# Kernel optimization log

Hardware: AMD Instinct MI355X
Metric: run time of the kernel (lower is better)

Reference implementation:

```python
import jax, jax.numpy as jnp
import numpy as np

ROW = COL = 8   # unfold tile size
KS = 5          # gaussian raster kernel size
C1 = 6          # high-freq feature split

def conv2d(x, w, b=None, pad=0):
    y = jax.lax.conv_general_dilated(x, w, (1, 1), [(pad, pad), (pad, pad)],
                                     dimension_numbers=('NCHW', 'OIHW', 'NCHW'))
    if b is not None:
        y = y + b[None, :, None, None]
    return y

def unfold_tiles(x, r, c):
    # non-overlapping Unfold(kernel=(r,c), stride=(r,c)) -> [B*L, C, r, c]
    B, C, H, W = x.shape
    x = x.reshape(B, C, H // r, r, W // c, c).transpose(0, 2, 4, 1, 3, 5)
    return x.reshape(B * (H // r) * (W // c), C, r, c)

def fold_tiles(t, B, C, H, W, r, c):
    t = t.reshape(B, H // r, W // c, C, r, c).transpose(0, 3, 1, 4, 2, 5)
    return t.reshape(B, C, H, W)

def setup_inputs() -> dict:
    key = jax.random.key(0)
    ks = jax.random.split(key, 16)
    B, NF, H, W, P = 32, 48, 128, 128, 81
    inp = {
        'ms': jax.random.normal(ks[0], (B, 4, 32, 32), jnp.float32),
        'feat': jax.random.normal(ks[1], (B, NF, H, W), jnp.float32),
        'V': jax.random.normal(ks[2], (B, NF, H, W), jnp.float32),
        'logits_raw': jax.random.normal(ks[3], (B, P, H, W), jnp.float32),
        'sigma_x': jax.random.uniform(ks[4], (P,), jnp.float32, 0.2, 3.0),
        'sigma_y': jax.random.uniform(ks[5], (P,), jnp.float32, 0.2, 3.0),
        'opacity': jax.random.uniform(ks[6], (P,), jnp.float32, 0.1, 1.0),
        'rho': jax.random.uniform(ks[7], (P,), jnp.float32, -0.9, 0.9),
        'w_v2': jax.random.normal(ks[8], (42, 42, 1, 1), jnp.float32) * 0.05,
        'w_fine': jax.random.normal(ks[9], (4, NF, 3, 3), jnp.float32) * 0.05,
        'b_fine': jax.random.normal(ks[10], (4,), jnp.float32) * 0.05,
        'w_res': jax.random.normal(ks[11], (4, NF, 1, 1), jnp.float32) * 0.05,
        'b_res': jax.random.normal(ks[12], (4,), jnp.float32) * 0.05,
    }
    return inp

def reference(ms, feat, V, logits_raw, sigma_x, sigma_y, opacity, rho,
              w_v2, w_fine, b_fine, w_res, b_res):
    B, nf, H, W = feat.shape
    # soft class assignment (gumbel_softmax tau=1, zero-noise deterministic surrogate)
    logits = jax.nn.softmax(logits_raw, axis=1)
    feat1, lr_feat = feat[:, :C1], feat[:, C1:]
    V1, V2 = V[:, :C1], V[:, C1:]
    # H,W are already multiples of ROW/COL -> bicubic-to-same-size is identity
    uf = unfold_tiles(feat1, ROW, COL)        # [B*L, c1, 8, 8]
    ul = unfold_tiles(logits, ROW, COL)       # [B*L, P, 8, 8]
    uv1 = unfold_tiles(V1, ROW, COL)          # [B*L, c1, 8, 8]
    # weighted gaussian params per in-tile position, averaged over all tiles
    pm = ul.reshape(ul.shape[0], ul.shape[1], -1).mean(axis=0)   # [P, 64]
    wsx = sigma_x @ pm; wsy = sigma_y @ pm                       # [64]
    wop = opacity @ pm; wr = rho @ pm                            # [64]
    # 2x2 covariance per point, analytic inverse
    a = wsx ** 2; bcv = wr * wsx * wsy; d = wsy ** 2
    det = a * d - bcv ** 2
    i00 = d / det; i01 = -bcv / det; i11 = a / det
    ax = jnp.linspace(-5.0, 5.0, KS)
    xx = ax[:, None]; yy = ax[None, :]
    z = -0.5 * (i00[:, None, None] * xx ** 2 + 2.0 * i01[:, None, None] * xx * yy
                + i11[:, None, None] * yy ** 2)
    kern = jnp.exp(z) / (2.0 * jnp.pi * jnp.sqrt(det))[:, None, None]   # [64, KS, KS]
    kern = kern / kern.max(axis=(-2, -1), keepdims=True)
    kern = kern * wop[:, None, None]
    # splat: place each point's kernel centered at its grid position in the 8x8 tile
    pad = KS // 2
    ii = jnp.arange(ROW * COL) // COL
    jj = jnp.arange(ROW * COL) % COL
    canvas = jnp.zeros((ROW + 2 * pad, COL + 2 * pad), kern.dtype)
    place = jax.vmap(lambda k, i, j: jax.lax.dynamic_update_slice(canvas, k, (i, j)))
    K = place(kern, ii, jj)[:, pad:pad + ROW, pad:pad + COL]             # [64, 8, 8]
    colors = uf.reshape(uf.shape[0], C1, ROW * COL)                      # [N, c1, 64]
    rendered = jnp.einsum('ncp,phw->nchw', colors, K) * uv1              # modulate by V1
    hr = fold_tiles(rendered, B, C1, H, W, ROW, COL)                     # [B, c1, H, W]
    # squeeze-style channel attention on low branch, modulated by V2
    gap = lr_feat.mean(axis=(2, 3), keepdims=True)
    attn = jax.nn.sigmoid(conv2d(gap, w_v2))
    lr_mod = lr_feat * attn * V2
    out_feat = jnp.concatenate([hr, lr_mod], axis=1)                     # [B, n_feats, H, W]
    up_ms = jax.image.resize(ms, (B, ms.shape[1], H, W), method='bilinear')
    out = conv2d(out_feat, w_fine, b_fine, pad=1) + conv2d(feat, w_res, b_res) + up_ms
    return out
```

## Files before the change

### kernel.cpp

```cpp
#include <hip/hip_runtime.h>

#define NBATCH 32
#define NFEAT 48
#define C1c 6
#define LRC 42
#define HH 128
#define WW 128
#define HWSZ 16384
#define NP 81
#define NQ 64

#define OFF_PM   0
#define OFF_GAP  5184
#define OFF_K    6528
#define OFF_ATTN 10624
#define OFF_WB   11968
#define OFF_HR   14272

__global__ __launch_bounds__(256) void k_phase1(const float* __restrict__ logits,
                                                const float* __restrict__ feat,
                                                const float* __restrict__ ms,
                                                const float* __restrict__ w_res,
                                                const float* __restrict__ b_fine,
                                                const float* __restrict__ b_res,
                                                float* __restrict__ part,
                                                float* __restrict__ gap,
                                                float* __restrict__ out) {
    int bid = blockIdx.x;
    int tid = threadIdx.x;
    if (bid < 1536) {
        int s   = bid >> 9;
        int idx = (bid & 511) * 256 + tid;
        int b   = idx >> 12;
        int pos = (idx & 4095) << 2;
        const float* base = logits + (((size_t)b * NP + 27 * s) << 14) + pos;
        float s0 = 0.f, s1 = 0.f, s2 = 0.f, s3 = 0.f;
        for (int p = 0; p < 27; ++p) {
            float4 v = *(const float4*)&base[(size_t)p << 14];
            s0 += __expf(v.x); s1 += __expf(v.y); s2 += __expf(v.z); s3 += __expf(v.w);
        }
        *(float4*)&part[((size_t)s << 19) + ((size_t)idx << 2)] =
            make_float4(s0, s1, s2, s3);
    } else {
        int gid = bid - 1536;
        int b = gid >> 4, strip = gid & 15;
        int row = (strip << 3) + (tid >> 5);
        int x0  = (tid & 31) << 2;
        int poff = (row << 7) + x0;
        int lane = tid & 63;
        const float* fb = feat + (((size_t)b * NFEAT) << 14);
        float a[4][4];
#pragma unroll
        for (int j = 0; j < 4; ++j)
#pragma unroll
            for (int o = 0; o < 4; ++o) a[j][o] = 0.f;
        for (int c = 0; c < NFEAT; ++c) {
            float4 f = *(const float4*)&fb[((size_t)c << 14) + poff];
            float wr0 = w_res[c], wr1 = w_res[NFEAT + c];
            float wr2 = w_res[2 * NFEAT + c], wr3 = w_res[3 * NFEAT + c];
            a[0][0] += wr0 * f.x; a[0][1] += wr1 * f.x; a[0][2] += wr2 * f.x; a[0][3] += wr3 * f.x;
            a[1][0] += wr0 * f.y; a[1][1] += wr1 * f.y; a[1][2] += wr2 * f.y; a[1][3] += wr3 * f.y;
            a[2][0] += wr0 * f.z; a[2][1] += wr1 * f.z; a[2][2] += wr2 * f.z; a[2][3] += wr3 * f.z;
            a[3][0] += wr0 * f.w; a[3][1] += wr1 * f.w; a[3][2] += wr2 * f.w; a[3][3] += wr3 * f.w;
            if (c >= C1c) {
                float s = (f.x + f.y) + (f.z + f.w);
                s += __shfl_xor(s, 1);  s += __shfl_xor(s, 2);  s += __shfl_xor(s, 4);
                s += __shfl_xor(s, 8);  s += __shfl_xor(s, 16); s += __shfl_xor(s, 32);
                if (lane == 0) atomicAdd(&gap[b * LRC + (c - C1c)], s);
            }
        }
        float syf = (row + 0.5f) * 0.25f - 0.5f;
        int y0i = (int)floorf(syf); float fy = syf - (float)y0i;
        int y0c = min(31, max(0, y0i)), y1c = min(31, max(0, y0i + 1));
        float fxv[4]; int x0v[4], x1v[4];
#pragma unroll
        for (int j = 0; j < 4; ++j) {
            float sxf = (x0 + j + 0.5f) * 0.25f - 0.5f;
            int x0i = (int)floorf(sxf);
            fxv[j] = sxf - (float)x0i;
            x0v[j] = min(31, max(0, x0i));
            x1v[j] = min(31, max(0, x0i + 1));
        }
#pragma unroll
        for (int o = 0; o < 4; ++o) {
            const float* mb = ms + ((size_t)(b * 4 + o) << 10);
            float addc = b_fine[o] + b_res[o];
            float res[4];
#pragma unroll
            for (int j = 0; j < 4; ++j) {
                float m00 = mb[(y0c << 5) + x0v[j]], m01 = mb[(y0c << 5) + x1v[j]];
                float m10 = mb[(y1c << 5) + x0v[j]], m11 = mb[(y1c << 5) + x1v[j]];
                float up = (m00 * (1.f - fxv[j]) + m01 * fxv[j]) * (1.f - fy)
                         + (m10 * (1.f - fxv[j]) + m11 * fxv[j]) * fy;
                res[j] = a[j][o] + addc + up;
            }
            *(float4*)&out[(((size_t)(b * 4 + o)) << 14) + poff] =
                make_float4(res[0], res[1], res[2], res[3]);
        }
    }
}

__global__ __launch_bounds__(256) void k_minv(const float* __restrict__ part,
                                              float* __restrict__ invbuf) {
    int idx = blockIdx.x * 256 + threadIdx.x;
    size_t o = (size_t)idx << 2;
    float4 p0 = *(const float4*)&part[o];
    float4 p1 = *(const float4*)&part[(1u << 19) + o];
    float4 p2 = *(const float4*)&part[(2u << 19) + o];
    *(float4*)&invbuf[o] = make_float4(1.f / (p0.x + p1.x + p2.x),
                                       1.f / (p0.y + p1.y + p2.y),
                                       1.f / (p0.z + p1.z + p2.z),
                                       1.f / (p0.w + p1.w + p2.w));
}

__global__ __launch_bounds__(256) void k_sm2(const float* __restrict__ logits,
                                             const float* __restrict__ invbuf,
                                             float* __restrict__ pm_sum) {
    int bid = blockIdx.x;
    int b = bid / NP, p = bid - b * NP;
    const float* base = logits + ((size_t)(b * NP + p) << 14);
    const float* ib   = invbuf + ((size_t)b << 14);
    int tid = threadIdx.x;
    int r0 = tid >> 5, xt = tid & 31;
    float a0 = 0.f, a1 = 0.f, a2 = 0.f, a3 = 0.f;
    int off = (r0 << 7) + (xt << 2);
#pragma unroll 4
    for (int k = 0; k < 16; ++k) {
        int o2 = off + k * 1024;
        float4 l4 = *(const float4*)&base[o2];
        float4 i4 = *(const float4*)&ib[o2];
        a0 += __expf(l4.x) * i4.x;
        a1 += __expf(l4.y) * i4.y;
        a2 += __expf(l4.z) * i4.z;
        a3 += __expf(l4.w) * i4.w;
    }
#pragma unroll
    for (int m = 2; m <= 16; m <<= 1) {
        a0 += __shfl_xor(a0, m); a1 += __shfl_xor(a1, m);
        a2 += __shfl_xor(a2, m); a3 += __shfl_xor(a3, m);
    }
    if (xt < 2) {
        int qb = p * NQ + (r0 << 3) + ((xt & 1) << 2);
        atomicAdd(&pm_sum[qb + 0], a0);
        atomicAdd(&pm_sum[qb + 1], a1);
        atomicAdd(&pm_sum[qb + 2], a2);
        atomicAdd(&pm_sum[qb + 3], a3);
    }
}

__global__ __launch_bounds__(256) void k_small(const float* __restrict__ pm_sum,
                                               const float* __restrict__ gap_sum,
                                               const float* __restrict__ sigx,
                                               const float* __restrict__ sigy,
                                               const float* __restrict__ opac,
                                               const float* __restrict__ rho,
                                               const float* __restrict__ w_v2,
                                               const float* __restrict__ w_fine,
                                               const float* __restrict__ w_res,
                                               float* __restrict__ Kmat,
                                               float* __restrict__ attn,
                                               float* __restrict__ wbuf) {
    int tid = threadIdx.x;
    if (tid < 64) {
        int q = tid;
        float wsx = 0.f, wsy = 0.f, wop = 0.f, wr = 0.f;
        for (int p = 0; p < NP; ++p) {
            float pv = pm_sum[p * NQ + q] * (1.f / 8192.f);
            wsx += sigx[p] * pv;
            wsy += sigy[p] * pv;
            wop += opac[p] * pv;
            wr  += rho[p]  * pv;
        }
        float a = wsx * wsx, d = wsy * wsy, bc = wr * wsx * wsy;
        float det = a * d - bc * bc;
        float i00 = d / det, i01 = -bc / det, i11 = a / det;
        int iq = q >> 3, jq = q & 7;
        for (int h = 0; h < 8; ++h)
            for (int w = 0; w < 8; ++w) {
                int ki = h - iq + 2, kj = w - jq + 2;
                float val = 0.f;
                if (ki >= 0 && ki < 5 && kj >= 0 && kj < 5) {
                    float xx = -5.f + 2.5f * ki, yy = -5.f + 2.5f * kj;
                    val = wop * __expf(-0.5f * (i00 * xx * xx + 2.f * i01 * xx * yy + i11 * yy * yy));
                }
                Kmat[(q << 6) + (h << 3) + w] = val;
            }
    }
    for (int i = tid; i < NBATCH * LRC; i += 256) {
        int b = i / LRC, co = i % LRC;
        float s = 0.f;
        for (int ci = 0; ci < LRC; ++ci) s += w_v2[co * LRC + ci] * gap_sum[b * LRC + ci];
        s *= (1.f / 16384.f);
        attn[i] = 1.f / (1.f + __expf(-s));
    }
    for (int i = tid; i < NFEAT * 48; i += 256) {
        int c = i / 48, j = i - c * 48;
        float v = 0.f;
        if (j < 36) v = w_fine[(j / 9) * (NFEAT * 9) + c * 9 + (j % 9)];
        else if (j < 40) v = w_res[(j - 36) * NFEAT + c];
        wbuf[i] = v;
    }
}

__global__ __launch_bounds__(256) void k_hr(const float* __restrict__ feat,
                                            const float* __restrict__ V,
                                            const float* __restrict__ Kmat,
                                            float* __restrict__ hrbuf) {
    __shared__ __align__(16) float lK[4096];
    __shared__ __align__(16) float lF[2 * 16 * 128];
    int bid = blockIdx.x;
    int b   = bid / 24;
    int r   = bid - b * 24;
    int strip = r / 3;
    int ch  = (r - strip * 3) * 2;
    int y0  = strip << 4;
    int tid = threadIdx.x;
    {
        const float4* ks = (const float4*)Kmat;
        float4* kd = (float4*)lK;
        for (int i = tid; i < 1024; i += 256) kd[i] = ks[i];
        float4* fd = (float4*)lF;
        const float* fb = feat + (((size_t)b * NFEAT + ch) << 14) + (y0 << 7);
        for (int i = tid; i < 1024; i += 256) {
            int c = i >> 9, rem = i & 511;
            fd[i] = *(const float4*)&fb[((size_t)c << 14) + (rem << 2)];
        }
    }
    __syncthreads();
    int tile = tid >> 3, hrow = tid & 7;
    int tr = tile >> 4, tx = tile & 15;
    float acc[2][8];
#pragma unroll
    for (int c = 0; c < 2; ++c)
#pragma unroll
        for (int j = 0; j < 8; ++j) acc[c][j] = 0.f;
    int fbase = (tr << 3) * 128 + (tx << 3);
    for (int q = 0; q < 64; ++q) {
        int iq = q >> 3, jq = q & 7;
        const float4 k0 = *(const float4*)&lK[(q << 6) + (hrow << 3)];
        const float4 k1 = *(const float4*)&lK[(q << 6) + (hrow << 3) + 4];
#pragma unroll
        for (int c = 0; c < 2; ++c) {
            float col = lF[(c << 11) + fbase + (iq << 7) + jq];
            acc[c][0] += col * k0.x; acc[c][1] += col * k0.y;
            acc[c][2] += col * k0.z; acc[c][3] += col * k0.w;
            acc[c][4] += col * k1.x; acc[c][5] += col * k1.y;
            acc[c][6] += col * k1.z; acc[c][7] += col * k1.w;
        }
    }
    int y = y0 + (tr << 3) + hrow;
#pragma unroll
    for (int c = 0; c < 2; ++c) {
        const float4* vp = (const float4*)(V + (((size_t)b * NFEAT + ch + c) << 14) + ((size_t)y << 7) + (tx << 3));
        float4 v0 = vp[0], v1 = vp[1];
        float4 r0, r1;
        r0.x = acc[c][0] * v0.x; r0.y = acc[c][1] * v0.y; r0.z = acc[c][2] * v0.z; r0.w = acc[c][3] * v0.w;
        r1.x = acc[c][4] * v1.x; r1.y = acc[c][5] * v1.y; r1.z = acc[c][6] * v1.z; r1.w = acc[c][7] * v1.w;
        float4* op = (float4*)(hrbuf + (((size_t)b * C1c + ch + c) << 14) + ((size_t)y << 7) + (tx << 3));
        op[0] = r0; op[1] = r1;
    }
}

#define CHN 6
__global__ __launch_bounds__(512, 4) void k_conv(const float* __restrict__ feat,
                                                 const float* __restrict__ V,
                                                 const float* __restrict__ wbuf,
                                                 const float* __restrict__ hrbuf,
                                                 const float* __restrict__ attn,
                                                 float* __restrict__ out) {
    __shared__ float s_in[2][CHN][18 * 40];
    int bid0 = blockIdx.x;
    int rid  = (bid0 & 7) * 128 + (bid0 >> 3);
    int b    = rid >> 5;
    int t32  = rid & 31;
    int ty0  = (t32 >> 2) << 4;
    int tx0  = (t32 & 3) << 5;
    int tid  = threadIdx.x;
    int grpu = __builtin_amdgcn_readfirstlane(tid >> 8);
    int ct   = tid & 255;
    int rp   = ct >> 5;
    int j    = ct & 31;
    int gx   = tx0 + j;
    int gy0  = ty0 + 2 * rp;
    int cbase = (2 * rp) * 40 + 3 + j;

    int srow = tid >> 5, scol = tid & 31;
    int sg = ((ty0 + srow) << 7) + tx0 + scol;
    int sl = (srow + 1) * 40 + 4 + scol;

    bool hhas = tid < 100;
    int rr, cc;
    if (tid < 34)      { rr = 0;        cc = tid; }
    else if (tid < 68) { rr = 17;       cc = tid - 34; }
    else if (tid < 84) { rr = tid - 67; cc = 0; }
    else               { rr = tid - 83; cc = 33; }
    int hsy = ty0 - 1 + rr, hsx = tx0 - 1 + cc;
    float hfm = (hsy >= 0 && hsy < HH && hsx >= 0 && hsx < WW) ? 1.f : 0.f;
    int hoff = (min(HH - 1, max(0, hsy)) << 7) + min(WW - 1, max(0, hsx));
    int hlds = rr * 40 + 3 + cc;

    const float* atb = attn + b * LRC;
    float a0[4] = {0.f, 0.f, 0.f, 0.f};
    float a1[4] = {0.f, 0.f, 0.f, 0.f};
    float rA[CHN], rB[CHN], rHA[CHN], rHB[CHN], amv[CHN];

#pragma unroll
    for (int k = 0; k < CHN; ++k) {
        const float* hs = hrbuf + (((size_t)(b * C1c + k)) << 14);
        rA[k]  = hs[sg];
        rHA[k] = hhas ? hs[hoff] : 0.f;
    }
#pragma unroll
    for (int k = 0; k < CHN; ++k) {
        s_in[0][k][sl] = rA[k];
        if (hhas) s_in[0][k][hlds] = rHA[k] * hfm;
    }
    int cur = 0;
    for (int t = 0; t < 8; ++t) {
        __syncthreads();
        if (t < 7) {
            int c0 = CHN * (t + 1);
#pragma unroll
            for (int k = 0; k < CHN; ++k) {
                int c = c0 + k;
                const float* fs = feat + (((size_t)(b * NFEAT + c)) << 14);
                const float* vs = V    + (((size_t)(b * NFEAT + c)) << 14);
                rA[k] = fs[sg];
                rB[k] = vs[sg];
                amv[k] = atb[c - C1c];
                rHA[k] = hhas ? fs[hoff] : 0.f;
                rHB[k] = hhas ? vs[hoff] : 0.f;
            }
        }
        int c0c = CHN * t;
        for (int k = 0; k < 3; ++k) {
            int slot = 3 * grpu + k;
            int c = c0c + slot;
            const float* wc = wbuf + c * 48;
            const float* sp = &s_in[cur][slot][cbase];
            float t00 = sp[0],   t01 = sp[1],   t02 = sp[2];
            float t10 = sp[40],  t11 = sp[41],  t12 = sp[42];
            float t20 = sp[80],  t21 = sp[81],  t22 = sp[82];
            float t30 = sp[120], t31 = sp[121], t32 = sp[122];
#pragma unroll
            for (int o = 0; o < 4; ++o) {
                float w0 = wc[o * 9 + 0], w1 = wc[o * 9 + 1], w2 = wc[o * 9 + 2];
                float w3 = wc[o * 9 + 3], w4 = wc[o * 9 + 4], w5 = wc[o * 9 + 5];
                float w6 = wc[o * 9 + 6], w7 = wc[o * 9 + 7], w8 = wc[o * 9 + 8];
                a0[o] += w0 * t00 + w1 * t01 + w2 * t02
                       + w3 * t10 + w4 * t11 + w5 * t12
                       + w6 * t20 + w7 * t21 + w8 * t22;
                a1[o] += w0 * t10 + w1 * t11 + w2 * t12
                       + w3 * t20 + w4 * t21 + w5 * t22
                       + w6 * t30 + w7 * t31 + w8 * t32;
            }
        }
        if (t < 7) {
            int nxt = cur ^ 1;
#pragma unroll
            for (int k = 0; k < CHN; ++k) {
                s_in[nxt][k][sl] = rA[k] * rB[k] * amv[k];
                if (hhas) s_in[nxt][k][hlds] = rHA[k] * rHB[k] * (amv[k] * hfm);
            }
        }
        cur ^= 1;
    }
    __syncthreads();
    float* sm = &s_in[0][0][0];
    int p0 = (2 * rp) * 32 + j, p1 = p0 + 32;
    if (grpu == 1) {
#pragma unroll
        for (int o = 0; o < 4; ++o) { sm[o * 512 + p0] = a0[o]; sm[o * 512 + p1] = a1[o]; }
    }
    __syncthreads();
    if (grpu == 0) {
#pragma unroll
        for (int o = 0; o < 4; ++o) {
            size_t obase = ((size_t)(b * 4 + o)) << 14;
            float* op0 = out + obase + (gy0 << 7) + gx;
            float* op1 = out + obase + ((gy0 + 1) << 7) + gx;
            *op0 = *op0 + a0[o] + sm[o * 512 + p0];
            *op1 = *op1 + a1[o] + sm[o * 512 + p1];
        }
    }
}

extern "C" void kernel_launch(void* const* d_in, const int* in_sizes, int n_in,
                              void* d_out, int out_size, void* d_ws, size_t ws_size,
                              hipStream_t stream) {
    (void)in_sizes; (void)n_in; (void)out_size; (void)ws_size;
    const float* ms     = (const float*)d_in[0];
    const float* feat   = (const float*)d_in[1];
    const float* V      = (const float*)d_in[2];
    const float* logits = (const float*)d_in[3];
    const float* sigx   = (const float*)d_in[4];
    const float* sigy   = (const float*)d_in[5];
    const float* opac   = (const float*)d_in[6];
    const float* rho    = (const float*)d_in[7];
    const float* w_v2   = (const float*)d_in[8];
    const float* w_fine = (const float*)d_in[9];
    const float* b_fine = (const float*)d_in[10];
    const float* w_res  = (const float*)d_in[11];
    const float* b_res  = (const float*)d_in[12];
    float* ws  = (float*)d_ws;
    float* out = (float*)d_out;
    float* part = ws + OFF_HR;
    float* inv  = ws + OFF_HR + 1572864;

    hipMemsetAsync(ws + OFF_PM, 0, (size_t)(NP * NQ + NBATCH * LRC) * sizeof(float), stream);
    k_phase1<<<1536 + 512, 256, 0, stream>>>(logits, feat, ms, w_res, b_fine, b_res,
                                             part, ws + OFF_GAP, out);
    k_minv<<<512, 256, 0, stream>>>(part, inv);
    k_sm2<<<NBATCH * NP, 256, 0, stream>>>(logits, inv, ws + OFF_PM);
    k_small<<<1, 256, 0, stream>>>(ws + OFF_PM, ws + OFF_GAP, sigx, sigy, opac, rho, w_v2,
                                   w_fine, w_res, ws + OFF_K, ws + OFF_ATTN, ws + OFF_WB);
    k_hr<<<768, 256, 0, stream>>>(feat, V, ws + OFF_K, ws + OFF_HR);
    k_conv<<<1024, 512, 0, stream>>>(feat, V, ws + OFF_WB, ws + OFF_HR, ws + OFF_ATTN, out);
}
```

Measured before the change: 207.5 us.

## Split softmax denominator pass into six class chunks with four loads in flight

Result: slower. 214.3 us (+3.3%).

```diff
diff --git a/kernel.cpp b/kernel.cpp
--- a/kernel.cpp
+++ b/kernel.cpp
@@ -28,21 +28,35 @@
                                                 float* __restrict__ out) {
     int bid = blockIdx.x;
     int tid = threadIdx.x;
-    if (bid < 1536) {
-        int s   = bid >> 9;
-        int idx = (bid & 511) * 256 + tid;
-        int b   = idx >> 12;
-        int pos = (idx & 4095) << 2;
-        const float* base = logits + (((size_t)b * NP + 27 * s) << 14) + pos;
-        float s0 = 0.f, s1 = 0.f, s2 = 0.f, s3 = 0.f;
-        for (int p = 0; p < 27; ++p) {
-            float4 v = *(const float4*)&base[(size_t)p << 14];
-            s0 += __expf(v.x); s1 += __expf(v.y); s2 += __expf(v.z); s3 += __expf(v.w);
-        }
-        *(float4*)&part[((size_t)s << 19) + ((size_t)idx << 2)] =
-            make_float4(s0, s1, s2, s3);
+    if (bid < 768) {
+        int s = bid >> 7;
+        int w = bid & 127;
+        int b = w >> 2;
+        int posb = (w & 3) << 10;
+        int pstart = (s < 3) ? s * 14 : 42 + (s - 3) * 13;
+        int pcnt   = (s < 3) ? 14 : 13;
+        const float4* lg4 = (const float4*)logits;
+        float4 A0 = make_float4(0.f, 0.f, 0.f, 0.f);
+        float4 A1 = A0, A2 = A0, A3 = A0;
+        for (int i = 0; i < pcnt; ++i) {
+            const float4* bp = lg4 + (((size_t)(b * NP + pstart + i)) << 12) + posb;
+            float4 va = bp[tid];
+            float4 vb = bp[tid + 256];
+            float4 vc = bp[tid + 512];
+            float4 vd = bp[tid + 768];
+            asm volatile("" :: "v"(va.x), "v"(vb.x), "v"(vc.x), "v"(vd.x));
+            A0.x += __expf(va.x); A0.y += __expf(va.y); A0.z += __expf(va.z); A0.w += __expf(va.w);
+            A1.x += __expf(vb.x); A1.y += __expf(vb.y); A1.z += __expf(vb.z); A1.w += __expf(vb.w);
+            A2.x += __expf(vc.x); A2.y += __expf(vc.y); A2.z += __expf(vc.z); A2.w += __expf(vc.w);
+            A3.x += __expf(vd.x); A3.y += __expf(vd.y); A3.z += __expf(vd.z); A3.w += __expf(vd.w);
+        }
+        float4* pp = (float4*)part + (size_t)s * 131072 + ((size_t)w << 10) + tid;
+        pp[0]   = A0;
+        pp[256] = A1;
+        pp[512] = A2;
+        pp[768] = A3;
     } else {
-        int gid = bid - 1536;
+        int gid = bid - 768;
         int b = gid >> 4, strip = gid & 15;
         int row = (strip << 3) + (tid >> 5);
         int x0  = (tid & 31) << 2;
@@ -100,17 +114,19 @@
     }
 }
 
-__global__ __launch_bounds__(256) void k_minv(const float* __restrict__ part,
-                                              float* __restrict__ invbuf) {
+__global__ __launch_bounds__(256) void k_minv(float* __restrict__ part) {
     int idx = blockIdx.x * 256 + threadIdx.x;
-    size_t o = (size_t)idx << 2;
-    float4 p0 = *(const float4*)&part[o];
-    float4 p1 = *(const float4*)&part[(1u << 19) + o];
-    float4 p2 = *(const float4*)&part[(2u << 19) + o];
-    *(float4*)&invbuf[o] = make_float4(1.f / (p0.x + p1.x + p2.x),
-                                       1.f / (p0.y + p1.y + p2.y),
-                                       1.f / (p0.z + p1.z + p2.z),
-                                       1.f / (p0.w + p1.w + p2.w));
+    float4* p4 = (float4*)part;
+    float4 s0 = p4[idx];
+    float4 s1 = p4[idx + 131072];
+    float4 s2 = p4[idx + 262144];
+    float4 s3 = p4[idx + 393216];
+    float4 s4 = p4[idx + 524288];
+    float4 s5 = p4[idx + 655360];
+    p4[idx] = make_float4(1.f / (s0.x + s1.x + s2.x + s3.x + s4.x + s5.x),
+                          1.f / (s0.y + s1.y + s2.y + s3.y + s4.y + s5.y),
+                          1.f / (s0.z + s1.z + s2.z + s3.z + s4.z + s5.z),
+                          1.f / (s0.w + s1.w + s2.w + s3.w + s4.w + s5.w));
 }
 
 __global__ __launch_bounds__(256) void k_sm2(const float* __restrict__ logits,
@@ -405,13 +421,12 @@
     float* ws  = (float*)d_ws;
     float* out = (float*)d_out;
     float* part = ws + OFF_HR;
-    float* inv  = ws + OFF_HR + 1572864;
 
     hipMemsetAsync(ws + OFF_PM, 0, (size_t)(NP * NQ + NBATCH * LRC) * sizeof(float), stream);
-    k_phase1<<<1536 + 512, 256, 0, stream>>>(logits, feat, ms, w_res, b_fine, b_res,
-                                             part, ws + OFF_GAP, out);
-    k_minv<<<512, 256, 0, stream>>>(part, inv);
-    k_sm2<<<NBATCH * NP, 256, 0, stream>>>(logits, inv, ws + OFF_PM);
+    k_phase1<<<768 + 512, 256, 0, stream>>>(logits, feat, ms, w_res, b_fine, b_res,
+                                            part, ws + OFF_GAP, out);
+    k_minv<<<512, 256, 0, stream>>>(part);
+    k_sm2<<<NBATCH * NP, 256, 0, stream>>>(logits, part, ws + OFF_PM);
     k_small<<<1, 256, 0, stream>>>(ws + OFF_PM, ws + OFF_GAP, sigx, sigy, opac, rho, w_v2,
                                    w_fine, w_res, ws + OFF_K, ws + OFF_ATTN, ws + OFF_WB);
     k_hr<<<768, 256, 0, stream>>>(feat, V, ws + OFF_K, ws + OFF_HR);
```
